# Performance work log

Hardware: AMD Instinct MI355X
Metric: run time of the kernel (lower is better)

## Reference

```python
import jax, jax.numpy as jnp
import numpy as np
from jax import lax

EPS = 1e-5
K = 32
S1, S2 = 512, 256


def bn_relu(x, gamma, beta, axes):
    # BatchNorm in training mode (batch statistics, biased variance) + ReLU.
    mean = jnp.mean(x, axis=axes, keepdims=True)
    var = jnp.var(x, axis=axes, keepdims=True)
    return jax.nn.relu((x - mean) * lax.rsqrt(var + EPS) * gamma + beta)


def fps(xyz, s):
    # Farthest point sampling, deterministic start at index 0. xyz: [N,3] -> [s] indices
    N = xyz.shape[0]
    def body(carry, _):
        dist, far = carry
        d = jnp.sum((xyz - xyz[far]) ** 2, axis=-1)
        dist = jnp.minimum(dist, d)
        return (dist, jnp.argmax(dist).astype(jnp.int32)), far
    init = (jnp.full((N,), 1e10, xyz.dtype), jnp.int32(0))
    _, idx = lax.scan(body, init, None, length=s)
    return idx


def sample_and_knn_group(s, k, coords, features):
    # coords: [B,N,3], features: [B,N,D]
    fps_idx = jax.vmap(lambda c: fps(c, s))(coords)                      # [B,s]
    new_xyz = jnp.take_along_axis(coords, fps_idx[..., None], axis=1)   # [B,s,3]
    new_feat = jnp.take_along_axis(features, fps_idx[..., None], axis=1)  # [B,s,D]
    # squared euclidean distances [B,s,N]
    d2 = (jnp.sum(new_xyz ** 2, -1)[..., None]
          - 2.0 * jnp.einsum('bsc,bnc->bsn', new_xyz, coords)
          + jnp.sum(coords ** 2, -1)[:, None, :])
    _, knn_idx = lax.top_k(-d2, k)                                       # [B,s,k]
    grouped = jax.vmap(lambda f, i: f[i])(features, knn_idx)             # [B,s,k,D]
    rel = grouped - new_feat[:, :, None, :]
    agg = jnp.concatenate([rel, jnp.broadcast_to(new_feat[:, :, None, :], rel.shape)], axis=-1)  # [B,s,k,2D]
    return new_xyz, agg


def sg_block(s, coords, feats, w1, cb1, g1, b1, w2, cb2, g2, b2):
    new_xyz, agg = sample_and_knn_group(s, K, coords, feats)
    h = bn_relu(jnp.einsum('bskc,oc->bsko', agg, w1) + cb1, g1, b1, (0, 1, 2))
    h = bn_relu(jnp.einsum('bskc,oc->bsko', h, w2) + cb2, g2, b2, (0, 1, 2))
    return new_xyz, jnp.max(h, axis=2)  # max over k neighbors -> [B,s,O]


def setup_inputs() -> dict:
    key = jax.random.key(0)
    ks = jax.random.split(key, 8)
    B, N = 16, 2048
    sc = 0.05
    return {
        'x': jax.random.normal(ks[0], (B, 3, N), jnp.float32),
        'emb_w1': jax.random.normal(ks[1], (64, 3), jnp.float32) * sc,
        'emb_g1': jnp.ones((64,), jnp.float32), 'emb_b1': jnp.zeros((64,), jnp.float32),
        'emb_w2': jax.random.normal(ks[2], (64, 64), jnp.float32) * sc,
        'emb_g2': jnp.ones((64,), jnp.float32), 'emb_b2': jnp.zeros((64,), jnp.float32),
        'sg1_w1': jax.random.normal(ks[3], (128, 128), jnp.float32) * sc,
        'sg1_cb1': jnp.zeros((128,), jnp.float32),
        'sg1_g1': jnp.ones((128,), jnp.float32), 'sg1_b1': jnp.zeros((128,), jnp.float32),
        'sg1_w2': jax.random.normal(ks[4], (128, 128), jnp.float32) * sc,
        'sg1_cb2': jnp.zeros((128,), jnp.float32),
        'sg1_g2': jnp.ones((128,), jnp.float32), 'sg1_b2': jnp.zeros((128,), jnp.float32),
        'sg2_w1': jax.random.normal(ks[5], (512, 256), jnp.float32) * sc,
        'sg2_cb1': jnp.zeros((512,), jnp.float32),
        'sg2_g1': jnp.ones((512,), jnp.float32), 'sg2_b1': jnp.zeros((512,), jnp.float32),
        'sg2_w2': jax.random.normal(ks[6], (512, 512), jnp.float32) * sc,
        'sg2_cb2': jnp.zeros((512,), jnp.float32),
        'sg2_g2': jnp.ones((512,), jnp.float32), 'sg2_b2': jnp.zeros((512,), jnp.float32),
    }


def reference(x, emb_w1, emb_g1, emb_b1, emb_w2, emb_g2, emb_b2,
              sg1_w1, sg1_cb1, sg1_g1, sg1_b1, sg1_w2, sg1_cb2, sg1_g2, sg1_b2,
              sg2_w1, sg2_cb1, sg2_g1, sg2_b1, sg2_w2, sg2_cb2, sg2_g2, sg2_b2):
    xyz = jnp.transpose(x, (0, 2, 1))  # [B,N,3]
    f = bn_relu(jnp.einsum('bnc,oc->bno', xyz, emb_w1), emb_g1, emb_b1, (0, 1))   # [B,N,64]
    f = bn_relu(jnp.einsum('bnc,oc->bno', f, emb_w2), emb_g2, emb_b2, (0, 1))
    xyz1, f1 = sg_block(S1, xyz, f, sg1_w1, sg1_cb1, sg1_g1, sg1_b1,
                        sg1_w2, sg1_cb2, sg1_g2, sg1_b2)   # [B,512,128]
    _, f2 = sg_block(S2, xyz1, f1, sg2_w1, sg2_cb1, sg2_g1, sg2_b1,
                     sg2_w2, sg2_cb2, sg2_g2, sg2_b2)      # [B,256,512]
    return jnp.transpose(f2, (0, 2, 1))  # [B,512,256] to match torch [B,C,s]
```

## Files before the change

kernel.cpp:

```cpp
#include <hip/hip_runtime.h>
#include <hip/hip_bf16.h>

#define EPS_BN 1e-5f
constexpr int BB = 16, NN = 2048, SS1 = 512, SS2 = 256, KNb = 32;

typedef short bf16x8 __attribute__((ext_vector_type(8)));
typedef float f32x4 __attribute__((ext_vector_type(4)));

__device__ inline float bflo(unsigned u) { return __uint_as_float(u << 16); }
__device__ inline float bfhi(unsigned u) { return __uint_as_float(u & 0xffff0000u); }
__device__ inline unsigned short f2bf_bits(float v) {
  __hip_bfloat16 h = __float2bfloat16(v);
  return *reinterpret_cast<unsigned short*>(&h);
}
__device__ inline unsigned fmono(float v) {
  int b = __float_as_int(v);
  return (unsigned)(b ^ ((b >> 31) | 0x80000000));
}
__device__ inline unsigned bn2(unsigned u, float s0, float h0, float s1, float h1) {
  float v0 = fmaxf(bflo(u) * s0 + h0, 0.f);
  float v1 = fmaxf(bfhi(u) * s1 + h1, 0.f);
  return (unsigned)f2bf_bits(v0) | ((unsigned)f2bf_bits(v1) << 16);
}

template <int CTRL>
__device__ inline void dpp_step_min(unsigned& hi, unsigned& lo) {
  unsigned hs = (unsigned)__builtin_amdgcn_update_dpp((int)hi, (int)hi, CTRL, 0xF, 0xF, false);
  unsigned ls = (unsigned)__builtin_amdgcn_update_dpp((int)lo, (int)lo, CTRL, 0xF, 0xF, false);
  bool take = (hs < hi) || (hs == hi && ls < lo);
  hi = take ? hs : hi; lo = take ? ls : lo;
}
template <int CTRL>
__device__ inline void dpp_step_maxv_minidx(unsigned& hi, unsigned& lo) {
  unsigned hs = (unsigned)__builtin_amdgcn_update_dpp((int)hi, (int)hi, CTRL, 0xF, 0xF, false);
  unsigned ls = (unsigned)__builtin_amdgcn_update_dpp((int)lo, (int)lo, CTRL, 0xF, 0xF, false);
  bool take = (hs > hi) || (hs == hi && ls < lo);
  hi = take ? hs : hi; lo = take ? ls : lo;
}
__device__ inline void dpp_chain_min(unsigned& hi, unsigned& lo) {
  dpp_step_min<0x111>(hi, lo); dpp_step_min<0x112>(hi, lo);
  dpp_step_min<0x114>(hi, lo); dpp_step_min<0x118>(hi, lo);
  dpp_step_min<0x142>(hi, lo); dpp_step_min<0x143>(hi, lo);
}
__device__ inline void dpp_chain_maxv_minidx(unsigned& hi, unsigned& lo) {
  dpp_step_maxv_minidx<0x111>(hi, lo); dpp_step_maxv_minidx<0x112>(hi, lo);
  dpp_step_maxv_minidx<0x114>(hi, lo); dpp_step_maxv_minidx<0x118>(hi, lo);
  dpp_step_maxv_minidx<0x142>(hi, lo); dpp_step_maxv_minidx<0x143>(hi, lo);
}
__device__ inline int dpp_reduce_min_idx(unsigned hi, unsigned lo) {
  dpp_chain_min(hi, lo);
  return __builtin_amdgcn_readlane((int)lo, 63);
}

__global__ void k_transpose(const float* __restrict__ x, float* __restrict__ xyz) {
  int idx = blockIdx.x * blockDim.x + threadIdx.x;
  if (idx >= BB * NN * 3) return;
  int c = idx % 3; int n = (idx / 3) % NN; int b = idx / (3 * NN);
  xyz[idx] = x[((size_t)b * 3 + c) * NN + n];
}

__global__ void k_emb1(const float* __restrict__ xyz, const float* __restrict__ w,
                       float* __restrict__ out) {
  int idx = blockIdx.x * blockDim.x + threadIdx.x;
  if (idx >= BB * NN * 64) return;
  int o = idx & 63; int pt = idx >> 6;
  const float* p = xyz + (size_t)pt * 3;
  const float* wr = w + o * 3;
  out[idx] = p[0] * wr[0] + p[1] * wr[1] + p[2] * wr[2];
}

__global__ void k_emb2(const float* __restrict__ fin, const float* __restrict__ w,
                       float* __restrict__ out) {
  int idx = blockIdx.x * blockDim.x + threadIdx.x;
  if (idx >= BB * NN * 64) return;
  int o = idx & 63; int pt = idx >> 6;
  const float* f = fin + (size_t)pt * 64;
  const float* wr = w + o * 64;
  float acc = 0.f;
#pragma unroll
  for (int c = 0; c < 64; c++) acc += f[c] * wr[c];
  out[idx] = acc;
}

__global__ __launch_bounds__(256) void k_stats_co(const float* __restrict__ d,
                                                  double* __restrict__ rsum,
                                                  double* __restrict__ rsq) {
  __shared__ float ls[64], lq[64];
  int t = threadIdx.x;
  if (t < 64) { ls[t] = 0.f; lq[t] = 0.f; }
  __syncthreads();
  size_t base = (size_t)blockIdx.x * 8192 + t * 4;
  float a0 = 0, a1 = 0, a2 = 0, a3 = 0, q0 = 0, q1 = 0, q2 = 0, q3 = 0;
  for (int it = 0; it < 8; it++) {
    float4 v = *(const float4*)(d + base + (size_t)it * 1024);
    a0 += v.x; q0 += v.x * v.x;
    a1 += v.y; q1 += v.y * v.y;
    a2 += v.z; q2 += v.z * v.z;
    a3 += v.w; q3 += v.w * v.w;
  }
  int c0 = (t * 4) & 63;
  atomicAdd(&ls[c0], a0); atomicAdd(&lq[c0], q0);
  atomicAdd(&ls[c0 + 1], a1); atomicAdd(&lq[c0 + 1], q1);
  atomicAdd(&ls[c0 + 2], a2); atomicAdd(&lq[c0 + 2], q2);
  atomicAdd(&ls[c0 + 3], a3); atomicAdd(&lq[c0 + 3], q3);
  __syncthreads();
  if (t < 64) {
    int rep = blockIdx.x & 63;
    atomicAdd(&rsum[(size_t)rep * 64 + t], (double)ls[t]);
    atomicAdd(&rsq[(size_t)rep * 64 + t], (double)lq[t]);
  }
}

__global__ void k_normrelu(float* __restrict__ data, const float* __restrict__ scale,
                           const float* __restrict__ shift, int total, int O) {
  int idx = blockIdx.x * blockDim.x + threadIdx.x;
  if (idx >= total) return;
  int o = idx % O;
  data[idx] = fmaxf(data[idx] * scale[o] + shift[o], 0.f);
}

template <int N>
__global__ __launch_bounds__(256, 1) void k_fps_mw(const float* __restrict__ xyz, int S,
                                                   int* __restrict__ fpsidx,
                                                   float* __restrict__ newxyz) {
  constexpr int PPL = N / 256;
  int b = blockIdx.x; int t = threadIdx.x;
  int w = t >> 6;
  __shared__ float4 sxyz[N];
  __shared__ unsigned combH[2][4], combL[2][4];
  float px[PPL], py[PPL], pz[PPL], ds[PPL];
#pragma unroll
  for (int r = 0; r < PPL; r++) {
    int i = r * 256 + t;
    size_t base = ((size_t)b * N + i) * 3;
    float xx = xyz[base], yy = xyz[base + 1], zz = xyz[base + 2];
    px[r] = xx; py[r] = yy; pz[r] = zz;
    float ox = xx, oy = yy, oz = zz;
    asm volatile("" : "+v"(ox), "+v"(oy), "+v"(oz));
    float4 o4 = {ox, oy, oz, 0.f};
    sxyz[i] = o4;
    ds[r] = 1e10f;
  }
  __syncthreads();
  int far = 0; int p = 0;
  for (int it = 0; it < S; it++) {
    float4 f4 = sxyz[far];
    float fx = f4.x, fy = f4.y, fz = f4.z;
    if (t == 0) {
      fpsidx[b * S + it] = far;
      size_t ob = ((size_t)b * S + it) * 3;
      newxyz[ob] = fx; newxyz[ob + 1] = fy; newxyz[ob + 2] = fz;
    }
    float mm0 = -1.f, mm1 = -1.f, mm2 = -1.f, mm3 = -1.f;
#pragma unroll
    for (int r = 0; r < PPL; r++) {
      float dx = px[r] - fx, dy = py[r] - fy, dz = pz[r] - fz;
      float d = dx * dx + dy * dy + dz * dz;
      float nd = d < ds[r] ? d : ds[r];
      ds[r] = nd;
      if ((r & 3) == 0) mm0 = nd > mm0 ? nd : mm0;
      else if ((r & 3) == 1) mm1 = nd > mm1 ? nd : mm1;
      else if ((r & 3) == 2) mm2 = nd > mm2 ? nd : mm2;
      else mm3 = nd > mm3 ? nd : mm3;
    }
    float m = fmaxf(fmaxf(mm0, mm1), fmaxf(mm2, mm3));
    int cand[PPL];
#pragma unroll
    for (int r = 0; r < PPL; r++) cand[r] = (ds[r] == m) ? (r * 256 + t) : 0x7fffffff;
#pragma unroll
    for (int st = PPL / 2; st > 0; st >>= 1)
#pragma unroll
      for (int r = 0; r < st; r++) cand[r] = cand[r] < cand[r + st] ? cand[r] : cand[r + st];
    unsigned hi = __float_as_uint(m);
    unsigned lo = (unsigned)cand[0];
    dpp_chain_maxv_minidx(hi, lo);
    unsigned rh = (unsigned)__builtin_amdgcn_readlane((int)hi, 63);
    unsigned rl = (unsigned)__builtin_amdgcn_readlane((int)lo, 63);
    combH[p][w] = rh;
    combL[p][w] = rl;
    __syncthreads();
    unsigned bh = combH[p][0], bl = combL[p][0];
#pragma unroll
    for (int ww = 1; ww < 4; ww++) {
      unsigned oh = combH[p][ww], ol = combL[p][ww];
      bool take = (oh > bh) || (oh == bh && ol < bl);
      bh = take ? oh : bh; bl = take ? ol : bl;
    }
    far = (int)bl;
    p ^= 1;
  }
}

template <int N, int S>
__global__ __launch_bounds__(64, 1) void k_knn_wave(const float* __restrict__ pts,
                                                    const float* __restrict__ ctr,
                                                    int* __restrict__ knn) {
  constexpr int PPL = N / 64;
  int blk = blockIdx.x; int lane = threadIdx.x;
  int b = blk / S;
  float cx = ctr[(size_t)blk * 3], cy = ctr[(size_t)blk * 3 + 1], cz = ctr[(size_t)blk * 3 + 2];
  float cn = cx * cx + cy * cy + cz * cz;
  float d2[PPL];
#pragma unroll
  for (int r = 0; r < PPL; r++) {
    int i = r * 64 + lane;
    size_t pb = ((size_t)b * N + i) * 3;
    float xx = pts[pb], yy = pts[pb + 1], zz = pts[pb + 2];
    d2[r] = cn - 2.f * (cx * xx + cy * yy + cz * zz) + (xx * xx + yy * yy + zz * zz);
  }
  for (int kk = 0; kk < KNb; kk++) {
    float a0 = d2[0], a1 = d2[1], a2 = d2[2], a3 = d2[3];
#pragma unroll
    for (int r = 4; r < PPL; r += 4) {
      a0 = fminf(a0, d2[r]); a1 = fminf(a1, d2[r + 1]);
      a2 = fminf(a2, d2[r + 2]); a3 = fminf(a3, d2[r + 3]);
    }
    float m = fminf(fminf(a0, a1), fminf(a2, a3));
    int cand[PPL];
#pragma unroll
    for (int r = 0; r < PPL; r++) cand[r] = (d2[r] == m) ? (r * 64 + lane) : 0x7fffffff;
#pragma unroll
    for (int st = PPL / 2; st > 0; st >>= 1)
#pragma unroll
      for (int r = 0; r < st; r++) cand[r] = cand[r] < cand[r + st] ? cand[r] : cand[r + st];
    int widx = dpp_reduce_min_idx(fmono(m), (unsigned)cand[0]);
    if (lane == 0) knn[(size_t)blk * KNb + kk] = widx;
    int wr = widx >> 6, wl = widx & 63;
#pragma unroll
    for (int r = 0; r < PPL; r++) d2[r] = (r == wr && lane == wl) ? 3.4e38f : d2[r];
  }
}

__global__ void k_f2bf(const float* __restrict__ w, __hip_bfloat16* __restrict__ o, int n) {
  int i = blockIdx.x * blockDim.x + threadIdx.x;
  if (i < n) o[i] = __float2bfloat16(w[i]);
}

template <int D>
__global__ __launch_bounds__(256) void k_gather(const float* __restrict__ feat, int N,
                                                const int* __restrict__ fpsidx,
                                                const int* __restrict__ knn, int S,
                                                __hip_bfloat16* __restrict__ A) {
  int blk = blockIdx.x; int b = blk / S; int t = threadIdx.x;
  __shared__ float cf[D]; __shared__ int nbr[KNb];
  if (t < KNb) nbr[t] = knn[(size_t)blk * KNb + t];
  int center = fpsidx[blk];
  for (int c = t; c < D; c += 256) cf[c] = feat[((size_t)b * N + center) * D + c];
  __syncthreads();
  for (int i = t; i < KNb * D; i += 256) {
    int kk = i / D, c = i - kk * D;
    float v = feat[((size_t)b * N + nbr[kk]) * D + c];
    size_t row = (size_t)blk * KNb + kk;
    A[row * (2 * D) + c] = __float2bfloat16(v - cf[c]);
    A[row * (2 * D) + D + c] = __float2bfloat16(cf[c]);
  }
}

template <int K, int EPI, bool BNA>
__global__ __launch_bounds__(256) void k_mgemm(
    const __hip_bfloat16* __restrict__ A, const __hip_bfloat16* __restrict__ W,
    int N, int Mtiles, const float* __restrict__ bias,
    const float* __restrict__ bnsc, const float* __restrict__ bnsh,
    __hip_bfloat16* __restrict__ Hout,
    float* __restrict__ maxb, float* __restrict__ minb,
    double* __restrict__ rsum, double* __restrict__ rsq) {
  constexpr int SP = 40;
  int bm = blockIdx.x % Mtiles; int bn = blockIdx.x / Mtiles;
  int t = threadIdx.x; int w = t >> 6; int lane = t & 63;
  int wm = w & 1, wn = w >> 1; int quad = lane >> 4; int l15 = lane & 15;
  __shared__ short As[128 * SP];
  __shared__ short Ws[128 * SP];
  __shared__ float scs[BNA ? K : 1], shs[BNA ? K : 1];
  if constexpr (BNA) {
    for (int i = t; i < K; i += 256) { scs[i] = bnsc[i]; shs[i] = bnsh[i]; }
  }
  f32x4 acc[4][4];
  f32x4 zero = {0.f, 0.f, 0.f, 0.f};
#pragma unroll
  for (int i = 0; i < 4; i++)
#pragma unroll
    for (int j = 0; j < 4; j++) acc[i][j] = zero;

  int srow = t >> 2, sseg = t & 3;
  const short* Ag = (const short*)A;
  const short* Wg = (const short*)W;
  size_t arow0 = (size_t)bm * 128;
  size_t wrow0 = (size_t)bn * 128;

  for (int k0 = 0; k0 < K; k0 += 32) {
    __syncthreads();
    uint4 a0 = *(const uint4*)(Ag + (arow0 + srow) * K + k0 + sseg * 8);
    uint4 a1 = *(const uint4*)(Ag + (arow0 + srow + 64) * K + k0 + sseg * 8);
    uint4 b0 = *(const uint4*)(Wg + (wrow0 + srow) * K + k0 + sseg * 8);
    uint4 b1 = *(const uint4*)(Wg + (wrow0 + srow + 64) * K + k0 + sseg * 8);
    if constexpr (BNA) {
      int cb = k0 + sseg * 8;
      float s[8], h[8];
#pragma unroll
      for (int q = 0; q < 8; q++) { s[q] = scs[cb + q]; h[q] = shs[cb + q]; }
      a0.x = bn2(a0.x, s[0], h[0], s[1], h[1]);
      a0.y = bn2(a0.y, s[2], h[2], s[3], h[3]);
      a0.z = bn2(a0.z, s[4], h[4], s[5], h[5]);
      a0.w = bn2(a0.w, s[6], h[6], s[7], h[7]);
      a1.x = bn2(a1.x, s[0], h[0], s[1], h[1]);
      a1.y = bn2(a1.y, s[2], h[2], s[3], h[3]);
      a1.z = bn2(a1.z, s[4], h[4], s[5], h[5]);
      a1.w = bn2(a1.w, s[6], h[6], s[7], h[7]);
    }
    *(uint4*)(As + srow * SP + sseg * 8) = a0;
    *(uint4*)(As + (srow + 64) * SP + sseg * 8) = a1;
    *(uint4*)(Ws + srow * SP + sseg * 8) = b0;
    *(uint4*)(Ws + (srow + 64) * SP + sseg * 8) = b1;
    __syncthreads();
    bf16x8 af[4], bfr[4];
#pragma unroll
    for (int i = 0; i < 4; i++)
      af[i] = *(const bf16x8*)(As + (wm * 64 + i * 16 + l15) * SP + quad * 8);
#pragma unroll
    for (int j = 0; j < 4; j++)
      bfr[j] = *(const bf16x8*)(Ws + (wn * 64 + j * 16 + l15) * SP + quad * 8);
#pragma unroll
    for (int i = 0; i < 4; i++)
#pragma unroll
      for (int j = 0; j < 4; j++)
        acc[i][j] = __builtin_amdgcn_mfma_f32_16x16x32_bf16(af[i], bfr[j], acc[i][j], 0, 0, 0);
  }

  if constexpr (EPI == 0) {
    int rep = blockIdx.x & 63;
#pragma unroll
    for (int j = 0; j < 4; j++) {
      int col = bn * 128 + wn * 64 + j * 16 + l15;
      float bs = bias[col];
      float su = 0.f, sq = 0.f;
#pragma unroll
      for (int i = 0; i < 4; i++)
#pragma unroll
        for (int r = 0; r < 4; r++) {
          int row = bm * 128 + wm * 64 + i * 16 + quad * 4 + r;
          float v = acc[i][j][r] + bs;
          Hout[(size_t)row * N + col] = __float2bfloat16(v);
          su += v; sq += v * v;
        }
      atomicAdd(&rsum[(size_t)rep * N + col], (double)su);
      atomicAdd(&rsq[(size_t)rep * N + col], (double)sq);
    }
  } else {
    __shared__ float buf[128][33];
    for (int s = 0; s < 4; s++) {
      __syncthreads();
      if (wn == (s >> 1)) {
        int jb = 2 * (s & 1);
#pragma unroll
        for (int jj = 0; jj < 2; jj++) {
          int j = jb + jj;
          int lcol = jj * 16 + l15;
          float bs = bias[bn * 128 + s * 32 + lcol];
#pragma unroll
          for (int i = 0; i < 4; i++)
#pragma unroll
            for (int r = 0; r < 4; r++)
              buf[wm * 64 + i * 16 + quad * 4 + r][lcol] = acc[i][j][r] + bs;
        }
      }
      __syncthreads();
      if (t < 128) {
        int g = t >> 5, c = t & 31;
        float mx = -3.4e38f, mn = 3.4e38f, su = 0.f, sq = 0.f;
#pragma unroll
        for (int r = 0; r < 32; r++) {
          float v = buf[g * 32 + r][c];
          mx = fmaxf(mx, v); mn = fminf(mn, v);
          su += v; sq += v * v;
        }
        int col = bn * 128 + s * 32 + c;
        size_t gidx = (size_t)bm * 4 + g;
        maxb[gidx * N + col] = mx;
        minb[gidx * N + col] = mn;
        int rep = blockIdx.x & 63;
        atomicAdd(&rsum[(size_t)rep * N + col], (double)su);
        atomicAdd(&rsq[(size_t)rep * N + col], (double)sq);
      }
    }
  }
}

__global__ void k_finalize(const double* __restrict__ rsum, const double* __restrict__ rsq,
                           int O, int rows,
                           const float* __restrict__ gamma, const float* __restrict__ beta,
                           float* __restrict__ scale, float* __restrict__ shift) {
  int o = blockIdx.x * blockDim.x + threadIdx.x;
  if (o >= O) return;
  double s = 0, s2 = 0;
  for (int r = 0; r < 64; r++) { s += rsum[(size_t)r * O + o]; s2 += rsq[(size_t)r * O + o]; }
  double mean = s / rows;
  double var = s2 / rows - mean * mean;
  float sc = gamma[o] * rsqrtf((float)var + EPS_BN);
  scale[o] = sc; shift[o] = beta[o] - (float)mean * sc;
}

__global__ void k_final_feat(const float* __restrict__ maxb, const float* __restrict__ minb,
                             const float* __restrict__ scale, const float* __restrict__ shift,
                             float* __restrict__ out, int total, int O) {
  int idx = blockIdx.x * blockDim.x + threadIdx.x;
  if (idx >= total) return;
  int o = idx % O; float sc = scale[o];
  float sel = sc > 0.f ? maxb[idx] : minb[idx];
  out[idx] = fmaxf(sel * sc + shift[o], 0.f);
}

__global__ void k_final_out(const float* __restrict__ maxb, const float* __restrict__ minb,
                            const float* __restrict__ scale, const float* __restrict__ shift,
                            float* __restrict__ out) {
  int idx = blockIdx.x * blockDim.x + threadIdx.x;
  if (idx >= BB * SS2 * 512) return;
  int o = idx % 512; int si = (idx / 512) % SS2; int b = idx / (512 * SS2);
  float sc = scale[o];
  float sel = sc > 0.f ? maxb[idx] : minb[idx];
  out[((size_t)b * 512 + o) * SS2 + si] = fmaxf(sel * sc + shift[o], 0.f);
}

extern "C" void kernel_launch(void* const* d_in, const int* in_sizes, int n_in,
                              void* d_out, int out_size, void* d_ws, size_t ws_size,
                              hipStream_t stream) {
  const float* x       = (const float*)d_in[0];
  const float* emb_w1  = (const float*)d_in[1];
  const float* emb_g1  = (const float*)d_in[2];
  const float* emb_b1  = (const float*)d_in[3];
  const float* emb_w2  = (const float*)d_in[4];
  const float* emb_g2  = (const float*)d_in[5];
  const float* emb_b2  = (const float*)d_in[6];
  const float* sg1_w1  = (const float*)d_in[7];
  const float* sg1_cb1 = (const float*)d_in[8];
  const float* sg1_g1  = (const float*)d_in[9];
  const float* sg1_b1  = (const float*)d_in[10];
  const float* sg1_w2  = (const float*)d_in[11];
  const float* sg1_cb2 = (const float*)d_in[12];
  const float* sg1_g2  = (const float*)d_in[13];
  const float* sg1_b2  = (const float*)d_in[14];
  const float* sg2_w1  = (const float*)d_in[15];
  const float* sg2_cb1 = (const float*)d_in[16];
  const float* sg2_g1  = (const float*)d_in[17];
  const float* sg2_b1  = (const float*)d_in[18];
  const float* sg2_w2  = (const float*)d_in[19];
  const float* sg2_cb2 = (const float*)d_in[20];
  const float* sg2_g2  = (const float*)d_in[21];
  const float* sg2_b2  = (const float*)d_in[22];

  char* ws = (char*)d_ws;
  size_t off = 0;
  auto alloc = [&](size_t bytes) -> size_t {
    size_t cur = off; off += (bytes + 255) & ~(size_t)255; return cur;
  };
  float* xyz  = (float*)(ws + alloc((size_t)BB * NN * 3 * 4));
  float* fA   = (float*)(ws + alloc((size_t)BB * NN * 64 * 4));
  float* fB   = (float*)(ws + alloc((size_t)BB * NN * 64 * 4));
  float* f1   = (float*)(ws + alloc((size_t)BB * SS1 * 128 * 4));
  float* nx1  = (float*)(ws + alloc((size_t)BB * SS1 * 3 * 4));
  float* nx2  = (float*)(ws + alloc((size_t)BB * SS2 * 3 * 4));
  int* fps1   = (int*)(ws + alloc((size_t)BB * SS1 * 4));
  int* fps2   = (int*)(ws + alloc((size_t)BB * SS2 * 4));
  int* knn1   = (int*)(ws + alloc((size_t)BB * SS1 * KNb * 4));
  int* knn2   = (int*)(ws + alloc((size_t)BB * SS2 * KNb * 4));
  float* maxb = (float*)(ws + alloc((size_t)BB * SS2 * 512 * 4));
  float* minb = (float*)(ws + alloc((size_t)BB * SS2 * 512 * 4));
  float* scbuf = (float*)(ws + alloc((size_t)12 * 512 * 4));
  float* sc11 = scbuf + 4 * 512, *sh11 = scbuf + 5 * 512;
  float* sc12 = scbuf + 6 * 512, *sh12 = scbuf + 7 * 512;
  float* sc21 = scbuf + 8 * 512, *sh21 = scbuf + 9 * 512;
  float* sc22 = scbuf + 10 * 512, *sh22 = scbuf + 11 * 512;
  float* sc_e1 = scbuf + 0 * 512, *sh_e1 = scbuf + 1 * 512;
  float* sc_e2 = scbuf + 2 * 512, *sh_e2 = scbuf + 3 * 512;
  size_t statsz = (size_t)12 * 64 * 512 * 8;
  char* statz = ws + alloc(statsz);
  double* st = (double*)statz;
  double* rsA = st + 0 * 64 * 512, *rqA = st + 1 * 64 * 512;
  double* rsB = st + 2 * 64 * 512, *rqB = st + 3 * 64 * 512;
  double* rsC = st + 4 * 64 * 512, *rqC = st + 5 * 64 * 512;
  double* rsD = st + 6 * 64 * 512, *rqD = st + 7 * 64 * 512;
  double* rsE1 = st + 8 * 64 * 512, *rqE1 = st + 9 * 64 * 512;
  double* rsE2 = st + 10 * 64 * 512, *rqE2 = st + 11 * 64 * 512;
  __hip_bfloat16* wb11 = (__hip_bfloat16*)(ws + alloc(128 * 128 * 2));
  __hip_bfloat16* wb12 = (__hip_bfloat16*)(ws + alloc(128 * 128 * 2));
  __hip_bfloat16* wb21 = (__hip_bfloat16*)(ws + alloc(512 * 256 * 2));
  __hip_bfloat16* wb22 = (__hip_bfloat16*)(ws + alloc(512 * 512 * 2));
  __hip_bfloat16* Abuf = (__hip_bfloat16*)(ws + alloc((size_t)262144 * 128 * 2));
  __hip_bfloat16* Hbuf = (__hip_bfloat16*)(ws + alloc((size_t)131072 * 512 * 2));

  hipMemsetAsync(statz, 0, statsz, stream);

  const int thr = 256;
  k_transpose<<<(BB * NN * 3 + thr - 1) / thr, thr, 0, stream>>>(x, xyz);
  k_emb1<<<(BB * NN * 64 + thr - 1) / thr, thr, 0, stream>>>(xyz, emb_w1, fA);
  k_stats_co<<<256, 256, 0, stream>>>(fA, rsE1, rqE1);
  k_finalize<<<1, 64, 0, stream>>>(rsE1, rqE1, 64, BB * NN, emb_g1, emb_b1, sc_e1, sh_e1);
  k_normrelu<<<(BB * NN * 64 + thr - 1) / thr, thr, 0, stream>>>(fA, sc_e1, sh_e1, BB * NN * 64, 64);
  k_emb2<<<(BB * NN * 64 + thr - 1) / thr, thr, 0, stream>>>(fA, emb_w2, fB);
  k_stats_co<<<256, 256, 0, stream>>>(fB, rsE2, rqE2);
  k_finalize<<<1, 64, 0, stream>>>(rsE2, rqE2, 64, BB * NN, emb_g2, emb_b2, sc_e2, sh_e2);
  k_normrelu<<<(BB * NN * 64 + thr - 1) / thr, thr, 0, stream>>>(fB, sc_e2, sh_e2, BB * NN * 64, 64);

  k_f2bf<<<(128 * 128 + 255) / 256, 256, 0, stream>>>(sg1_w1, wb11, 128 * 128);
  k_f2bf<<<(128 * 128 + 255) / 256, 256, 0, stream>>>(sg1_w2, wb12, 128 * 128);
  k_f2bf<<<(512 * 256 + 255) / 256, 256, 0, stream>>>(sg2_w1, wb21, 512 * 256);
  k_f2bf<<<(512 * 512 + 255) / 256, 256, 0, stream>>>(sg2_w2, wb22, 512 * 512);

  k_fps_mw<NN><<<BB, 256, 0, stream>>>(xyz, SS1, fps1, nx1);
  k_knn_wave<NN, SS1><<<BB * SS1, 64, 0, stream>>>(xyz, nx1, knn1);

  k_gather<64><<<BB * SS1, 256, 0, stream>>>(fB, NN, fps1, knn1, SS1, Abuf);
  k_mgemm<128, 0, false><<<2048, 256, 0, stream>>>(Abuf, wb11, 128, 2048, sg1_cb1,
                                                   nullptr, nullptr, Hbuf,
                                                   nullptr, nullptr, rsA, rqA);
  k_finalize<<<1, 128, 0, stream>>>(rsA, rqA, 128, 262144, sg1_g1, sg1_b1, sc11, sh11);
  k_mgemm<128, 1, true><<<2048, 256, 0, stream>>>(Hbuf, wb12, 128, 2048, sg1_cb2,
                                                  sc11, sh11, nullptr,
                                                  maxb, minb, rsB, rqB);
  k_finalize<<<1, 128, 0, stream>>>(rsB, rqB, 128, 262144, sg1_g2, sg1_b2, sc12, sh12);
  k_final_feat<<<(BB * SS1 * 128 + thr - 1) / thr, thr, 0, stream>>>(maxb, minb, sc12, sh12,
                                                                     f1, BB * SS1 * 128, 128);

  k_fps_mw<SS1><<<BB, 256, 0, stream>>>(nx1, SS2, fps2, nx2);
  k_knn_wave<SS1, SS2><<<BB * SS2, 64, 0, stream>>>(nx1, nx2, knn2);

  k_gather<128><<<BB * SS2, 256, 0, stream>>>(f1, SS1, fps2, knn2, SS2, Abuf);
  k_mgemm<256, 0, false><<<1024 * 4, 256, 0, stream>>>(Abuf, wb21, 512, 1024, sg2_cb1,
                                                       nullptr, nullptr, Hbuf,
                                                       nullptr, nullptr, rsC, rqC);
  k_finalize<<<4, 128, 0, stream>>>(rsC, rqC, 512, 131072, sg2_g1, sg2_b1, sc21, sh21);
  k_mgemm<512, 1, true><<<1024 * 4, 256, 0, stream>>>(Hbuf, wb22, 512, 1024, sg2_cb2,
                                                      sc21, sh21, nullptr,
                                                      maxb, minb, rsD, rqD);
  k_finalize<<<4, 128, 0, stream>>>(rsD, rqD, 512, 131072, sg2_g2, sg2_b2, sc22, sh22);
  k_final_out<<<(BB * SS2 * 512 + thr - 1) / thr, thr, 0, stream>>>(maxb, minb, sc22, sh22,
                                                                    (float*)d_out);
}
```

Measured before the change: 1.339 ms.

## Fuse FPS, embedding, weight conversion and KNN into concurrent mega-kernels

Merges the transpose, first embedding layer with its statistics, both FPS stages (the second FPS reuses the first's sampled centers from LDS) and the weight bf16 conversions into one heterogeneous launch. Point-cloud KNN for stage 1 is fused with the second embedding layer and its statistics, and the BN+ReLU normalizations are folded into consumers (embedding 2 input, gather). The serial FPS blocks overlap with the bulk parallel work, which removes launch overheads and several full passes over the feature tensors. The risk is that FPS blocks hold CUs with launch_bounds(256,1) and large LDS while other blocks queue, and the mega-kernel's register/LDS footprint is set by its largest branch.

```diff
diff --git a/kernel.cpp b/kernel.cpp
--- a/kernel.cpp
+++ b/kernel.cpp
@@ -52,153 +52,253 @@
   return __builtin_amdgcn_readlane((int)lo, 63);
 }
 
-__global__ void k_transpose(const float* __restrict__ x, float* __restrict__ xyz) {
-  int idx = blockIdx.x * blockDim.x + threadIdx.x;
-  if (idx >= BB * NN * 3) return;
-  int c = idx % 3; int n = (idx / 3) % NN; int b = idx / (3 * NN);
-  xyz[idx] = x[((size_t)b * 3 + c) * NN + n];
-}
-
-__global__ void k_emb1(const float* __restrict__ xyz, const float* __restrict__ w,
-                       float* __restrict__ out) {
-  int idx = blockIdx.x * blockDim.x + threadIdx.x;
-  if (idx >= BB * NN * 64) return;
-  int o = idx & 63; int pt = idx >> 6;
-  const float* p = xyz + (size_t)pt * 3;
-  const float* wr = w + o * 3;
-  out[idx] = p[0] * wr[0] + p[1] * wr[1] + p[2] * wr[2];
-}
-
-__global__ void k_emb2(const float* __restrict__ fin, const float* __restrict__ w,
-                       float* __restrict__ out) {
-  int idx = blockIdx.x * blockDim.x + threadIdx.x;
-  if (idx >= BB * NN * 64) return;
-  int o = idx & 63; int pt = idx >> 6;
-  const float* f = fin + (size_t)pt * 64;
-  const float* wr = w + o * 64;
+__global__ __launch_bounds__(256, 1) void k_mega1(
+    const float* __restrict__ x, const float* __restrict__ emb_w1,
+    float* __restrict__ fA, double* __restrict__ rsE1, double* __restrict__ rqE1,
+    int* __restrict__ fps1, float* __restrict__ nx1,
+    int* __restrict__ fps2, float* __restrict__ nx2,
+    const float* __restrict__ w11f, __hip_bfloat16* __restrict__ wb11,
+    const float* __restrict__ w12f, __hip_bfloat16* __restrict__ wb12,
+    const float* __restrict__ w21f, __hip_bfloat16* __restrict__ wb21,
+    const float* __restrict__ w22f, __hip_bfloat16* __restrict__ wb22) {
+  int blk = blockIdx.x;
+  int t = threadIdx.x;
+  if (blk < BB) {
+    constexpr int PPL = NN / 256;
+    constexpr int PPL2 = SS1 / 256;
+    int b = blk; int w = t >> 6;
+    __shared__ float4 sxyz[NN];
+    __shared__ float4 c4[SS1];
+    __shared__ unsigned combH[2][4], combL[2][4];
+    float px[PPL], py[PPL], pz[PPL], ds[PPL];
+#pragma unroll
+    for (int r = 0; r < PPL; r++) {
+      int i = r * 256 + t;
+      float xx = x[(size_t)(b * 3 + 0) * NN + i];
+      float yy = x[(size_t)(b * 3 + 1) * NN + i];
+      float zz = x[(size_t)(b * 3 + 2) * NN + i];
+      px[r] = xx; py[r] = yy; pz[r] = zz;
+      float ox = xx, oy = yy, oz = zz;
+      asm volatile("" : "+v"(ox), "+v"(oy), "+v"(oz));
+      float4 o4 = {ox, oy, oz, 0.f};
+      sxyz[i] = o4;
+      ds[r] = 1e10f;
+    }
+    __syncthreads();
+    int far = 0; int p = 0;
+    for (int it = 0; it < SS1; it++) {
+      float4 f4 = sxyz[far];
+      float fx = f4.x, fy = f4.y, fz = f4.z;
+      if (t == 0) {
+        fps1[b * SS1 + it] = far;
+        size_t ob = ((size_t)b * SS1 + it) * 3;
+        nx1[ob] = fx; nx1[ob + 1] = fy; nx1[ob + 2] = fz;
+        c4[it] = f4;
+      }
+      float mm0 = -1.f, mm1 = -1.f, mm2 = -1.f, mm3 = -1.f;
+#pragma unroll
+      for (int r = 0; r < PPL; r++) {
+        float dx = px[r] - fx, dy = py[r] - fy, dz = pz[r] - fz;
+        float d = dx * dx + dy * dy + dz * dz;
+        float nd = d < ds[r] ? d : ds[r];
+        ds[r] = nd;
+        if ((r & 3) == 0) mm0 = nd > mm0 ? nd : mm0;
+        else if ((r & 3) == 1) mm1 = nd > mm1 ? nd : mm1;
+        else if ((r & 3) == 2) mm2 = nd > mm2 ? nd : mm2;
+        else mm3 = nd > mm3 ? nd : mm3;
+      }
+      float m = fmaxf(fmaxf(mm0, mm1), fmaxf(mm2, mm3));
+      int cand[PPL];
+#pragma unroll
+      for (int r = 0; r < PPL; r++) cand[r] = (ds[r] == m) ? (r * 256 + t) : 0x7fffffff;
+#pragma unroll
+      for (int st = PPL / 2; st > 0; st >>= 1)
+#pragma unroll
+        for (int r = 0; r < st; r++) cand[r] = cand[r] < cand[r + st] ? cand[r] : cand[r + st];
+      unsigned hi = __float_as_uint(m);
+      unsigned lo = (unsigned)cand[0];
+      dpp_chain_maxv_minidx(hi, lo);
+      unsigned rh = (unsigned)__builtin_amdgcn_readlane((int)hi, 63);
+      unsigned rl = (unsigned)__builtin_amdgcn_readlane((int)lo, 63);
+      combH[p][w] = rh; combL[p][w] = rl;
+      __syncthreads();
+      unsigned bh = combH[p][0], bl = combL[p][0];
+#pragma unroll
+      for (int ww = 1; ww < 4; ww++) {
+        unsigned oh = combH[p][ww], ol = combL[p][ww];
+        bool take = (oh > bh) || (oh == bh && ol < bl);
+        bh = take ? oh : bh; bl = take ? ol : bl;
+      }
+      far = (int)bl;
+      p ^= 1;
+    }
+    __syncthreads();
+    float qx[PPL2], qy[PPL2], qz[PPL2], es[PPL2];
+#pragma unroll
+    for (int r = 0; r < PPL2; r++) {
+      float4 v = c4[r * 256 + t];
+      qx[r] = v.x; qy[r] = v.y; qz[r] = v.z; es[r] = 1e10f;
+    }
+    int far2 = 0;
+    for (int it = 0; it < SS2; it++) {
+      float4 f4 = c4[far2];
+      float fx = f4.x, fy = f4.y, fz = f4.z;
+      if (t == 0) {
+        fps2[b * SS2 + it] = far2;
+        size_t ob = ((size_t)b * SS2 + it) * 3;
+        nx2[ob] = fx; nx2[ob + 1] = fy; nx2[ob + 2] = fz;
+      }
+      float mm0, mm1;
+      { float dx = qx[0] - fx, dy = qy[0] - fy, dz = qz[0] - fz;
+        float d = dx * dx + dy * dy + dz * dz;
+        float nd = d < es[0] ? d : es[0]; es[0] = nd; mm0 = nd; }
+      { float dx = qx[1] - fx, dy = qy[1] - fy, dz = qz[1] - fz;
+        float d = dx * dx + dy * dy + dz * dz;
+        float nd = d < es[1] ? d : es[1]; es[1] = nd; mm1 = nd; }
+      float m = fmaxf(mm0, mm1);
+      int c0 = (es[0] == m) ? t : 0x7fffffff;
+      int c1 = (es[1] == m) ? (256 + t) : 0x7fffffff;
+      int cnd = c0 < c1 ? c0 : c1;
+      unsigned hi = __float_as_uint(m), lo = (unsigned)cnd;
+      dpp_chain_maxv_minidx(hi, lo);
+      unsigned rh = (unsigned)__builtin_amdgcn_readlane((int)hi, 63);
+      unsigned rl = (unsigned)__builtin_amdgcn_readlane((int)lo, 63);
+      combH[p][w] = rh; combL[p][w] = rl;
+      __syncthreads();
+      unsigned bh = combH[p][0], bl = combL[p][0];
+#pragma unroll
+      for (int ww = 1; ww < 4; ww++) {
+        unsigned oh = combH[p][ww], ol = combL[p][ww];
+        bool take = (oh > bh) || (oh == bh && ol < bl);
+        bh = take ? oh : bh; bl = take ? ol : bl;
+      }
+      far2 = (int)bl;
+      p ^= 1;
+    }
+    return;
+  }
+  blk -= BB;
+  if (blk < 8192) {
+    __shared__ float ls[64], lq[64];
+    if (t < 64) { ls[t] = 0.f; lq[t] = 0.f; }
+    __syncthreads();
+    int o = t & 63;
+    int pt = blk * 4 + (t >> 6);
+    int b = pt >> 11, n = pt & (NN - 1);
+    float x0 = x[(size_t)(b * 3 + 0) * NN + n];
+    float x1 = x[(size_t)(b * 3 + 1) * NN + n];
+    float x2 = x[(size_t)(b * 3 + 2) * NN + n];
+    float v = x0 * emb_w1[o * 3] + x1 * emb_w1[o * 3 + 1] + x2 * emb_w1[o * 3 + 2];
+    fA[(size_t)pt * 64 + o] = v;
+    atomicAdd(&ls[o], v);
+    atomicAdd(&lq[o], v * v);
+    __syncthreads();
+    if (t < 64) {
+      int rep = blk & 63;
+      atomicAdd(&rsE1[(size_t)rep * 64 + t], (double)ls[t]);
+      atomicAdd(&rqE1[(size_t)rep * 64 + t], (double)lq[t]);
+    }
+    return;
+  }
+  blk -= 8192;
+  if (blk < 64) { int i = blk * 256 + t; wb11[i] = __float2bfloat16(w11f[i]); return; }
+  blk -= 64;
+  if (blk < 64) { int i = blk * 256 + t; wb12[i] = __float2bfloat16(w12f[i]); return; }
+  blk -= 64;
+  if (blk < 512) { int i = blk * 256 + t; wb21[i] = __float2bfloat16(w21f[i]); return; }
+  blk -= 512;
+  { int i = blk * 256 + t; wb22[i] = __float2bfloat16(w22f[i]); }
+}
+
+__global__ __launch_bounds__(256) void k_mega2(
+    const float* __restrict__ x, const float* __restrict__ nx1, int* __restrict__ knn1,
+    const float* __restrict__ fA, const float* __restrict__ sce1,
+    const float* __restrict__ she1, const float* __restrict__ w2,
+    float* __restrict__ fB, double* __restrict__ rsE2, double* __restrict__ rqE2) {
+  int blk = blockIdx.x; int t = threadIdx.x;
+  if (blk < 2048) {
+    constexpr int PPL = NN / 64;
+    int lane = t & 63;
+    int center = blk * 4 + (t >> 6);
+    int b = center >> 9;
+    float cx = nx1[(size_t)center * 3], cy = nx1[(size_t)center * 3 + 1],
+          cz = nx1[(size_t)center * 3 + 2];
+    float cn = cx * cx + cy * cy + cz * cz;
+    float d2[PPL];
+#pragma unroll
+    for (int r = 0; r < PPL; r++) {
+      int i = r * 64 + lane;
+      float xx = x[(size_t)(b * 3 + 0) * NN + i];
+      float yy = x[(size_t)(b * 3 + 1) * NN + i];
+      float zz = x[(size_t)(b * 3 + 2) * NN + i];
+      d2[r] = cn - 2.f * (cx * xx + cy * yy + cz * zz) + (xx * xx + yy * yy + zz * zz);
+    }
+    for (int kk = 0; kk < KNb; kk++) {
+      float a0 = d2[0], a1 = d2[1], a2 = d2[2], a3 = d2[3];
+#pragma unroll
+      for (int r = 4; r < PPL; r += 4) {
+        a0 = fminf(a0, d2[r]); a1 = fminf(a1, d2[r + 1]);
+        a2 = fminf(a2, d2[r + 2]); a3 = fminf(a3, d2[r + 3]);
+      }
+      float m = fminf(fminf(a0, a1), fminf(a2, a3));
+      int cand[PPL];
+#pragma unroll
+      for (int r = 0; r < PPL; r++) cand[r] = (d2[r] == m) ? (r * 64 + lane) : 0x7fffffff;
+#pragma unroll
+      for (int st = PPL / 2; st > 0; st >>= 1)
+#pragma unroll
+        for (int r = 0; r < st; r++) cand[r] = cand[r] < cand[r + st] ? cand[r] : cand[r + st];
+      int widx = dpp_reduce_min_idx(fmono(m), (unsigned)cand[0]);
+      if (lane == 0) knn1[(size_t)center * KNb + kk] = widx;
+      int wr = widx >> 6, wl = widx & 63;
+#pragma unroll
+      for (int r = 0; r < PPL; r++) d2[r] = (r == wr && lane == wl) ? 3.4e38f : d2[r];
+    }
+    return;
+  }
+  blk -= 2048;
+  __shared__ float wT[64][65];
+  __shared__ float fs[4][64];
+  __shared__ float ss[64], sq[64];
+#pragma unroll
+  for (int k = 0; k < 16; k++) {
+    int idx = k * 256 + t;
+    wT[idx & 63][idx >> 6] = w2[idx];
+  }
+  if (t < 64) { ss[t] = 0.f; sq[t] = 0.f; }
+  int pt0 = blk * 4;
+  {
+    float v = fA[(size_t)pt0 * 64 + t];
+    int c = t & 63;
+    v = fmaxf(v * sce1[c] + she1[c], 0.f);
+    fs[t >> 6][c] = v;
+  }
+  __syncthreads();
+  int o = t & 63, pq = t >> 6;
   float acc = 0.f;
-#pragma unroll
-  for (int c = 0; c < 64; c++) acc += f[c] * wr[c];
-  out[idx] = acc;
-}
-
-__global__ __launch_bounds__(256) void k_stats_co(const float* __restrict__ d,
-                                                  double* __restrict__ rsum,
-                                                  double* __restrict__ rsq) {
-  __shared__ float ls[64], lq[64];
-  int t = threadIdx.x;
-  if (t < 64) { ls[t] = 0.f; lq[t] = 0.f; }
-  __syncthreads();
-  size_t base = (size_t)blockIdx.x * 8192 + t * 4;
-  float a0 = 0, a1 = 0, a2 = 0, a3 = 0, q0 = 0, q1 = 0, q2 = 0, q3 = 0;
-  for (int it = 0; it < 8; it++) {
-    float4 v = *(const float4*)(d + base + (size_t)it * 1024);
-    a0 += v.x; q0 += v.x * v.x;
-    a1 += v.y; q1 += v.y * v.y;
-    a2 += v.z; q2 += v.z * v.z;
-    a3 += v.w; q3 += v.w * v.w;
-  }
-  int c0 = (t * 4) & 63;
-  atomicAdd(&ls[c0], a0); atomicAdd(&lq[c0], q0);
-  atomicAdd(&ls[c0 + 1], a1); atomicAdd(&lq[c0 + 1], q1);
-  atomicAdd(&ls[c0 + 2], a2); atomicAdd(&lq[c0 + 2], q2);
-  atomicAdd(&ls[c0 + 3], a3); atomicAdd(&lq[c0 + 3], q3);
+#pragma unroll 8
+  for (int c = 0; c < 64; c++) acc += fs[pq][c] * wT[c][o];
+  fB[(size_t)pt0 * 64 + t] = acc;
+  atomicAdd(&ss[o], acc);
+  atomicAdd(&sq[o], acc * acc);
   __syncthreads();
   if (t < 64) {
-    int rep = blockIdx.x & 63;
-    atomicAdd(&rsum[(size_t)rep * 64 + t], (double)ls[t]);
-    atomicAdd(&rsq[(size_t)rep * 64 + t], (double)lq[t]);
-  }
-}
-
-__global__ void k_normrelu(float* __restrict__ data, const float* __restrict__ scale,
-                           const float* __restrict__ shift, int total, int O) {
-  int idx = blockIdx.x * blockDim.x + threadIdx.x;
-  if (idx >= total) return;
-  int o = idx % O;
-  data[idx] = fmaxf(data[idx] * scale[o] + shift[o], 0.f);
-}
-
-template <int N>
-__global__ __launch_bounds__(256, 1) void k_fps_mw(const float* __restrict__ xyz, int S,
-                                                   int* __restrict__ fpsidx,
-                                                   float* __restrict__ newxyz) {
-  constexpr int PPL = N / 256;
-  int b = blockIdx.x; int t = threadIdx.x;
-  int w = t >> 6;
-  __shared__ float4 sxyz[N];
-  __shared__ unsigned combH[2][4], combL[2][4];
-  float px[PPL], py[PPL], pz[PPL], ds[PPL];
-#pragma unroll
-  for (int r = 0; r < PPL; r++) {
-    int i = r * 256 + t;
-    size_t base = ((size_t)b * N + i) * 3;
-    float xx = xyz[base], yy = xyz[base + 1], zz = xyz[base + 2];
-    px[r] = xx; py[r] = yy; pz[r] = zz;
-    float ox = xx, oy = yy, oz = zz;
-    asm volatile("" : "+v"(ox), "+v"(oy), "+v"(oz));
-    float4 o4 = {ox, oy, oz, 0.f};
-    sxyz[i] = o4;
-    ds[r] = 1e10f;
-  }
-  __syncthreads();
-  int far = 0; int p = 0;
-  for (int it = 0; it < S; it++) {
-    float4 f4 = sxyz[far];
-    float fx = f4.x, fy = f4.y, fz = f4.z;
-    if (t == 0) {
-      fpsidx[b * S + it] = far;
-      size_t ob = ((size_t)b * S + it) * 3;
-      newxyz[ob] = fx; newxyz[ob + 1] = fy; newxyz[ob + 2] = fz;
-    }
-    float mm0 = -1.f, mm1 = -1.f, mm2 = -1.f, mm3 = -1.f;
-#pragma unroll
-    for (int r = 0; r < PPL; r++) {
-      float dx = px[r] - fx, dy = py[r] - fy, dz = pz[r] - fz;
-      float d = dx * dx + dy * dy + dz * dz;
-      float nd = d < ds[r] ? d : ds[r];
-      ds[r] = nd;
-      if ((r & 3) == 0) mm0 = nd > mm0 ? nd : mm0;
-      else if ((r & 3) == 1) mm1 = nd > mm1 ? nd : mm1;
-      else if ((r & 3) == 2) mm2 = nd > mm2 ? nd : mm2;
-      else mm3 = nd > mm3 ? nd : mm3;
-    }
-    float m = fmaxf(fmaxf(mm0, mm1), fmaxf(mm2, mm3));
-    int cand[PPL];
-#pragma unroll
-    for (int r = 0; r < PPL; r++) cand[r] = (ds[r] == m) ? (r * 256 + t) : 0x7fffffff;
-#pragma unroll
-    for (int st = PPL / 2; st > 0; st >>= 1)
-#pragma unroll
-      for (int r = 0; r < st; r++) cand[r] = cand[r] < cand[r + st] ? cand[r] : cand[r + st];
-    unsigned hi = __float_as_uint(m);
-    unsigned lo = (unsigned)cand[0];
-    dpp_chain_maxv_minidx(hi, lo);
-    unsigned rh = (unsigned)__builtin_amdgcn_readlane((int)hi, 63);
-    unsigned rl = (unsigned)__builtin_amdgcn_readlane((int)lo, 63);
-    combH[p][w] = rh;
-    combL[p][w] = rl;
-    __syncthreads();
-    unsigned bh = combH[p][0], bl = combL[p][0];
-#pragma unroll
-    for (int ww = 1; ww < 4; ww++) {
-      unsigned oh = combH[p][ww], ol = combL[p][ww];
-      bool take = (oh > bh) || (oh == bh && ol < bl);
-      bh = take ? oh : bh; bl = take ? ol : bl;
-    }
-    far = (int)bl;
-    p ^= 1;
+    int rep = blk & 63;
+    atomicAdd(&rsE2[(size_t)rep * 64 + t], (double)ss[t]);
+    atomicAdd(&rqE2[(size_t)rep * 64 + t], (double)sq[t]);
   }
 }
 
 template <int N, int S>
-__global__ __launch_bounds__(64, 1) void k_knn_wave(const float* __restrict__ pts,
-                                                    const float* __restrict__ ctr,
-                                                    int* __restrict__ knn) {
+__global__ __launch_bounds__(256) void k_knn4(const float* __restrict__ pts,
+                                              const float* __restrict__ ctr,
+                                              int* __restrict__ knn) {
   constexpr int PPL = N / 64;
-  int blk = blockIdx.x; int lane = threadIdx.x;
-  int b = blk / S;
-  float cx = ctr[(size_t)blk * 3], cy = ctr[(size_t)blk * 3 + 1], cz = ctr[(size_t)blk * 3 + 2];
+  int lane = threadIdx.x & 63;
+  int center = blockIdx.x * 4 + (threadIdx.x >> 6);
+  int b = center / S;
+  float cx = ctr[(size_t)center * 3], cy = ctr[(size_t)center * 3 + 1],
+        cz = ctr[(size_t)center * 3 + 2];
   float cn = cx * cx + cy * cy + cz * cz;
   float d2[PPL];
 #pragma unroll
@@ -224,32 +324,34 @@
 #pragma unroll
       for (int r = 0; r < st; r++) cand[r] = cand[r] < cand[r + st] ? cand[r] : cand[r + st];
     int widx = dpp_reduce_min_idx(fmono(m), (unsigned)cand[0]);
-    if (lane == 0) knn[(size_t)blk * KNb + kk] = widx;
+    if (lane == 0) knn[(size_t)center * KNb + kk] = widx;
     int wr = widx >> 6, wl = widx & 63;
 #pragma unroll
     for (int r = 0; r < PPL; r++) d2[r] = (r == wr && lane == wl) ? 3.4e38f : d2[r];
   }
 }
 
-__global__ void k_f2bf(const float* __restrict__ w, __hip_bfloat16* __restrict__ o, int n) {
-  int i = blockIdx.x * blockDim.x + threadIdx.x;
-  if (i < n) o[i] = __float2bfloat16(w[i]);
-}
-
-template <int D>
+template <int D, bool BN>
 __global__ __launch_bounds__(256) void k_gather(const float* __restrict__ feat, int N,
                                                 const int* __restrict__ fpsidx,
                                                 const int* __restrict__ knn, int S,
+                                                const float* __restrict__ bnsc,
+                                                const float* __restrict__ bnsh,
                                                 __hip_bfloat16* __restrict__ A) {
   int blk = blockIdx.x; int b = blk / S; int t = threadIdx.x;
   __shared__ float cf[D]; __shared__ int nbr[KNb];
   if (t < KNb) nbr[t] = knn[(size_t)blk * KNb + t];
   int center = fpsidx[blk];
-  for (int c = t; c < D; c += 256) cf[c] = feat[((size_t)b * N + center) * D + c];
+  for (int c = t; c < D; c += 256) {
+    float v = feat[((size_t)b * N + center) * D + c];
+    if constexpr (BN) v = fmaxf(v * bnsc[c] + bnsh[c], 0.f);
+    cf[c] = v;
+  }
   __syncthreads();
   for (int i = t; i < KNb * D; i += 256) {
     int kk = i / D, c = i - kk * D;
     float v = feat[((size_t)b * N + nbr[kk]) * D + c];
+    if constexpr (BN) v = fmaxf(v * bnsc[c] + bnsh[c], 0.f);
     size_t row = (size_t)blk * KNb + kk;
     A[row * (2 * D) + c] = __float2bfloat16(v - cf[c]);
     A[row * (2 * D) + D + c] = __float2bfloat16(cf[c]);
@@ -452,7 +554,6 @@
   auto alloc = [&](size_t bytes) -> size_t {
     size_t cur = off; off += (bytes + 255) & ~(size_t)255; return cur;
   };
-  float* xyz  = (float*)(ws + alloc((size_t)BB * NN * 3 * 4));
   float* fA   = (float*)(ws + alloc((size_t)BB * NN * 64 * 4));
   float* fB   = (float*)(ws + alloc((size_t)BB * NN * 64 * 4));
   float* f1   = (float*)(ws + alloc((size_t)BB * SS1 * 128 * 4));
@@ -490,25 +591,15 @@
   hipMemsetAsync(statz, 0, statsz, stream);
 
   const int thr = 256;
-  k_transpose<<<(BB * NN * 3 + thr - 1) / thr, thr, 0, stream>>>(x, xyz);
-  k_emb1<<<(BB * NN * 64 + thr - 1) / thr, thr, 0, stream>>>(xyz, emb_w1, fA);
-  k_stats_co<<<256, 256, 0, stream>>>(fA, rsE1, rqE1);
+  k_mega1<<<9872, 256, 0, stream>>>(x, emb_w1, fA, rsE1, rqE1, fps1, nx1, fps2, nx2,
+                                    sg1_w1, wb11, sg1_w2, wb12, sg2_w1, wb21, sg2_w2, wb22);
   k_finalize<<<1, 64, 0, stream>>>(rsE1, rqE1, 64, BB * NN, emb_g1, emb_b1, sc_e1, sh_e1);
-  k_normrelu<<<(BB * NN * 64 + thr - 1) / thr, thr, 0, stream>>>(fA, sc_e1, sh_e1, BB * NN * 64, 64);
-  k_emb2<<<(BB * NN * 64 + thr - 1) / thr, thr, 0, stream>>>(fA, emb_w2, fB);
-  k_stats_co<<<256, 256, 0, stream>>>(fB, rsE2, rqE2);
+  k_mega2<<<10240, 256, 0, stream>>>(x, nx1, knn1, fA, sc_e1, sh_e1, emb_w2,
+                                     fB, rsE2, rqE2);
   k_finalize<<<1, 64, 0, stream>>>(rsE2, rqE2, 64, BB * NN, emb_g2, emb_b2, sc_e2, sh_e2);
-  k_normrelu<<<(BB * NN * 64 + thr - 1) / thr, thr, 0, stream>>>(fB, sc_e2, sh_e2, BB * NN * 64, 64);
-
-  k_f2bf<<<(128 * 128 + 255) / 256, 256, 0, stream>>>(sg1_w1, wb11, 128 * 128);
-  k_f2bf<<<(128 * 128 + 255) / 256, 256, 0, stream>>>(sg1_w2, wb12, 128 * 128);
-  k_f2bf<<<(512 * 256 + 255) / 256, 256, 0, stream>>>(sg2_w1, wb21, 512 * 256);
-  k_f2bf<<<(512 * 512 + 255) / 256, 256, 0, stream>>>(sg2_w2, wb22, 512 * 512);
-
-  k_fps_mw<NN><<<BB, 256, 0, stream>>>(xyz, SS1, fps1, nx1);
-  k_knn_wave<NN, SS1><<<BB * SS1, 64, 0, stream>>>(xyz, nx1, knn1);
-
-  k_gather<64><<<BB * SS1, 256, 0, stream>>>(fB, NN, fps1, knn1, SS1, Abuf);
+
+  k_gather<64, true><<<BB * SS1, 256, 0, stream>>>(fB, NN, fps1, knn1, SS1,
+                                                   sc_e2, sh_e2, Abuf);
   k_mgemm<128, 0, false><<<2048, 256, 0, stream>>>(Abuf, wb11, 128, 2048, sg1_cb1,
                                                    nullptr, nullptr, Hbuf,
                                                    nullptr, nullptr, rsA, rqA);
@@ -520,10 +611,10 @@
   k_final_feat<<<(BB * SS1 * 128 + thr - 1) / thr, thr, 0, stream>>>(maxb, minb, sc12, sh12,
                                                                      f1, BB * SS1 * 128, 128);
 
-  k_fps_mw<SS1><<<BB, 256, 0, stream>>>(nx1, SS2, fps2, nx2);
-  k_knn_wave<SS1, SS2><<<BB * SS2, 64, 0, stream>>>(nx1, nx2, knn2);
-
-  k_gather<128><<<BB * SS2, 256, 0, stream>>>(f1, SS1, fps2, knn2, SS2, Abuf);
+  k_knn4<SS1, SS2><<<BB * SS2 / 4, 256, 0, stream>>>(nx1, nx2, knn2);
+
+  k_gather<128, false><<<BB * SS2, 256, 0, stream>>>(f1, SS1, fps2, knn2, SS2,
+                                                     nullptr, nullptr, Abuf);
   k_mgemm<256, 0, false><<<1024 * 4, 256, 0, stream>>>(Abuf, wb21, 512, 1024, sg2_cb1,
                                                        nullptr, nullptr, Hbuf,
                                                        nullptr, nullptr, rsC, rqC);
```

After: 1.253 ms. -6.4%, faster.
